# Kernel optimization log

Hardware: AMD Instinct MI355X
Metric: run time of the kernel (lower is better)

The kernel has to match this reference:

```python
import jax, jax.numpy as jnp
import numpy as np

N = 50000   # nodes
D = 128     # hidden_dim
H = 8       # num_heads
DK = D // H # per-head dim
E = 1600000 # edges
L = 2       # n_layers
LN_EPS = 1e-5


def _layer_norm(x, g, b):
    m = jnp.mean(x, axis=-1, keepdims=True)
    v = jnp.mean(jnp.square(x - m), axis=-1, keepdims=True)
    return (x - m) * jax.lax.rsqrt(v + LN_EPS) * g + b


def _gt_layer(h, src, dst, Wq, bq, Wk, bk, Wv, bv, Wo, bo, W1, b1, W2, b2, g1, be1, g2, be2):
    n = h.shape[0]
    Q = (h @ Wq + bq).reshape(n, H, DK)
    K = (h @ Wk + bk).reshape(n, H, DK)
    V = (h @ Wv + bv).reshape(n, H, DK)
    # per-edge scaled dot-product score: K[src] . Q[dst]
    score = jnp.einsum('ehd,ehd->eh', K[src], Q[dst]) / np.sqrt(DK)
    score = jnp.exp(jnp.clip(score, -5.0, 5.0))            # [E,H]
    wV = jax.ops.segment_sum(V[src] * score[:, :, None], dst, num_segments=n)  # [N,H,DK]
    z = jax.ops.segment_sum(score, dst, num_segments=n)    # [N,H]
    attn = wV / (z[:, :, None] + 1e-6)                     # possible_empty-safe softmax
    h_att = attn.reshape(n, D) @ Wo + bo
    h = _layer_norm(h + h_att, g1, be1)                    # residual + LN
    ffn = jax.nn.relu(h @ W1 + b1) @ W2 + b2
    h = _layer_norm(h + ffn, g2, be2)                      # residual + LN
    return h


def setup_inputs() -> dict:
    key = jax.random.key(0)
    ks = jax.random.split(key, 16)
    s = 1.0 / np.sqrt(D)
    s2 = 1.0 / np.sqrt(2 * D)
    w = lambda k, shape, sc: jax.random.normal(k, shape, jnp.float32) * sc
    return {
        'h':   jax.random.normal(ks[0], (N, D), jnp.float32),
        'src': jax.random.randint(ks[1], (E,), 0, N),
        'dst': jax.random.randint(ks[2], (E,), 0, N),
        'Wq': w(ks[3], (L, D, D), s), 'bq': jnp.zeros((L, D), jnp.float32),
        'Wk': w(ks[4], (L, D, D), s), 'bk': jnp.zeros((L, D), jnp.float32),
        'Wv': w(ks[5], (L, D, D), s), 'bv': jnp.zeros((L, D), jnp.float32),
        'Wo': w(ks[6], (L, D, D), s), 'bo': jnp.zeros((L, D), jnp.float32),
        'W1': w(ks[7], (L, D, 2 * D), s), 'b1': jnp.zeros((L, 2 * D), jnp.float32),
        'W2': w(ks[8], (L, 2 * D, D), s2), 'b2': jnp.zeros((L, D), jnp.float32),
        'ln1_g': jnp.ones((L, D), jnp.float32), 'ln1_b': jnp.zeros((L, D), jnp.float32),
        'ln2_g': jnp.ones((L, D), jnp.float32), 'ln2_b': jnp.zeros((L, D), jnp.float32),
    }


def reference(h, src, dst, Wq, bq, Wk, bk, Wv, bv, Wo, bo, W1, b1, W2, b2, ln1_g, ln1_b, ln2_g, ln2_b):
    for l in range(L):
        h = _gt_layer(h, src, dst, Wq[l], bq[l], Wk[l], bk[l], Wv[l], bv[l],
                      Wo[l], bo[l], W1[l], b1[l], W2[l], b2[l],
                      ln1_g[l], ln1_b[l], ln2_g[l], ln2_b[l])
    return h
```

## Files before the change

kernel.cpp:

```cpp
#include <hip/hip_runtime.h>

#define NN 50000
#define DD 128
#define HH 8
#define EE 1600000
#define LL 2

typedef unsigned short u16;
typedef __attribute__((ext_vector_type(8))) __bf16 bf16x8;
typedef __attribute__((ext_vector_type(4))) float f32x4;
typedef __attribute__((ext_vector_type(2))) float f32x2;

__device__ __forceinline__ float bf2f(u16 u){
    return __uint_as_float(((unsigned int)u) << 16);
}
__device__ __forceinline__ u16 f2bf(float f){
    unsigned int x = __float_as_uint(f);
    x = x + 0x7fff + ((x >> 16) & 1);
    return (u16)(x >> 16);
}

__device__ __forceinline__ void async16(const u16* g, u16* l){
    __builtin_amdgcn_global_load_lds(
        (const __attribute__((address_space(1))) unsigned int*)(const void*)g,
        (__attribute__((address_space(3))) unsigned int*)(void*)l, 16, 0, 0);
}

#define FILL_SUB 128
#define PREP_BLOCKS (1024 + 6250 + 384 + 768)

__global__ __launch_bounds__(256) void prep_kernel(
        const int* __restrict__ dst, int* __restrict__ cnt,
        const float* __restrict__ h_in, u16* __restrict__ hb,
        const float* __restrict__ Wq, const float* __restrict__ Wk, const float* __restrict__ Wv,
        const float* __restrict__ bq, const float* __restrict__ bk, const float* __restrict__ bv,
        u16* __restrict__ WtQKV, float* __restrict__ bQKV,
        const float* __restrict__ Wo, const float* __restrict__ W1, const float* __restrict__ W2,
        u16* __restrict__ WtO, u16* __restrict__ WtF1, u16* __restrict__ WtF2){
    int b = blockIdx.x;
    if (b < 1024){
        int slice = b & 7;
        int sub = b >> 3;
        int lo = slice * (NN / 8), hi = lo + (NN / 8);
        for (int e = sub * 256 + threadIdx.x; e < EE; e += FILL_SUB * 256){
            int d = dst[e];
            if (d >= lo && d < hi) atomicAdd(&cnt[d], 1);
        }
        return;
    }
    b -= 1024;
    if (b < 6250){
        int i = b * 256 + threadIdx.x;
        if (i < NN * DD / 4){
            float4 v = ((const float4*)h_in)[i];
            ushort4 o;
            o.x = f2bf(v.x); o.y = f2bf(v.y); o.z = f2bf(v.z); o.w = f2bf(v.w);
            ((ushort4*)hb)[i] = o;
        }
        return;
    }
    b -= 6250;
    if (b < 384){
        int l = b / 192;
        int idx = (b % 192) * 256 + threadIdx.x;
        if (idx < 384 * 128){
            int n = idx >> 7, k = idx & 127;
            const float* W = (n < 128) ? Wq : (n < 256) ? Wk : Wv;
            int nc = n & 127;
            WtQKV[(size_t)l * 384 * 128 + idx] = f2bf(W[(size_t)l * 128 * 128 + k * 128 + nc]);
            if (k == 0){
                const float* bb = (n < 128) ? bq : (n < 256) ? bk : bv;
                bQKV[l * 384 + n] = bb[l * 128 + nc];
            }
        }
        return;
    }
    b -= 384;
    {
        int which = b / 256;
        int rem = b % 256;
        int l = rem / 128;
        int idx = (rem % 128) * 256 + threadIdx.x;
        const float* in; u16* out; int R, C;
        if (which == 0){ in = Wo; out = WtO; R = 128; C = 128; }
        else if (which == 1){ in = W1; out = WtF1; R = 128; C = 256; }
        else { in = W2; out = WtF2; R = 256; C = 128; }
        int total = R * C;
        if (idx < total){
            size_t mat = (size_t)l * total;
            int r = idx / C, c = idx % C;
            out[mat + (size_t)c * R + r] = f2bf(in[mat + idx]);
        }
    }
}

__global__ __launch_bounds__(1024) void scan_kernel(const int* __restrict__ cnt,
                                                    int* __restrict__ offs, int* __restrict__ cur){
    __shared__ int wsum[16];
    __shared__ int carry_s;
    __shared__ int ctot_s;
    int t = threadIdx.x, lane = t & 63, w = t >> 6;
    if (t == 0){ offs[0] = 0; cur[0] = 0; carry_s = 0; }
    __syncthreads();
    const int N4 = NN / 4;
    for (int base = 0; base < N4; base += 1024){
        int i4 = base + t;
        int4 x = (i4 < N4) ? ((const int4*)cnt)[i4] : make_int4(0, 0, 0, 0);
        int s1 = x.x, s2 = s1 + x.y, s3 = s2 + x.z, s4 = s3 + x.w;
        int v = s4;
        #pragma unroll
        for (int d = 1; d < 64; d <<= 1){ int u = __shfl_up(v, d); if (lane >= d) v += u; }
        if (lane == 63) wsum[w] = v;
        __syncthreads();
        if (t < 16){
            int sv = wsum[t];
            int iv = sv;
            #pragma unroll
            for (int d = 1; d < 16; d <<= 1){ int u = __shfl_up(iv, d); if (t >= d) iv += u; }
            wsum[t] = iv - sv;
            if (t == 15) ctot_s = iv;
        }
        __syncthreads();
        int excl = carry_s + wsum[w] + (v - s4);
        if (i4 < N4){
            int o = 4 * i4;
            offs[o + 1] = excl + s1;  cur[o + 1] = excl + s1;
            offs[o + 2] = excl + s2;  cur[o + 2] = excl + s2;
            offs[o + 3] = excl + s3;  cur[o + 3] = excl + s3;
            offs[o + 4] = excl + s4;  cur[o + 4] = excl + s4;
        }
        __syncthreads();
        if (t == 0) carry_s += ctot_s;
        __syncthreads();
    }
}

__global__ __launch_bounds__(256) void fill_kernel(const int* __restrict__ src, const int* __restrict__ dst,
                                                   int* __restrict__ cur, int* __restrict__ srcs){
    int slice = blockIdx.x & 7;
    int sub = blockIdx.x >> 3;
    int lo = slice * (NN / 8), hi = lo + (NN / 8);
    for (int e = sub * 256 + threadIdx.x; e < EE; e += FILL_SUB * 256){
        int d = dst[e];
        if (d >= lo && d < hi){
            int p = atomicAdd(&cur[d], 1);
            srcs[p] = src[e];
        }
    }
}

#define BM 128
#define LDC 136

__device__ __forceinline__ void stage_tile(const u16* __restrict__ A, const u16* __restrict__ Wt,
                                           u16* As, u16* Bs, int M, int K, int m0, int n0, int k0,
                                           int w, int lane){
    int lr = lane >> 3;
    int swz = ((lane & 7) ^ lr) * 8;
    #pragma unroll
    for (int p = 0; p < 4; p++){
        int s = p * 4 + w;
        int ga = m0 + s * 8 + lr;
        if (ga >= M) ga = M - 1;
        async16(A + (size_t)ga * K + k0 + swz, As + s * 512);
        async16(Wt + (size_t)(n0 + s * 8 + lr) * K + k0 + swz, Bs + s * 512);
    }
}

__device__ __forceinline__ void mfma_tiles(const u16* As, const u16* Bs, f32x4 (&acc)[4][4],
                                           int wm, int wn, int l15, int hi){
    #pragma unroll
    for (int ks = 0; ks < 2; ks++){
        bf16x8 a[4], b[4];
        int ca = ((ks * 4 + hi) ^ (l15 & 7)) * 8;
        #pragma unroll
        for (int i = 0; i < 4; i++){
            a[i] = *(const bf16x8*)(As + (wm * 64 + i * 16 + l15) * 64 + ca);
            b[i] = *(const bf16x8*)(Bs + (wn * 64 + i * 16 + l15) * 64 + ca);
        }
        #pragma unroll
        for (int mi = 0; mi < 4; mi++)
            #pragma unroll
            for (int ni = 0; ni < 4; ni++)
                acc[mi][ni] = __builtin_amdgcn_mfma_f32_16x16x32_bf16(a[mi], b[ni], acc[mi][ni], 0, 0, 0);
    }
}

#define GEMM_LOOP(K)                                                          \
    for (int k0 = 0; k0 < (K); k0 += 64){                                     \
        __syncthreads();                                                      \
        stage_tile(A, Wt, As, Bs, M, (K), m0, n0, k0, w, lane);               \
        asm volatile("s_waitcnt vmcnt(0)" ::: "memory");                      \
        __syncthreads();                                                      \
        mfma_tiles(As, Bs, acc, wm, wn, l15, hi);                             \
    }

__global__ __launch_bounds__(256) void gemm_qkv(const u16* __restrict__ A, const u16* __restrict__ Wt,
                                                const float* __restrict__ bias,
                                                u16* __restrict__ Qb, u16* __restrict__ Kb,
                                                unsigned char* __restrict__ Vb, int M){
    __shared__ __align__(16) char smem[128 * LDC * 2];
    u16* As = (u16*)smem;
    u16* Bs = As + 8192;
    u16* Cs = (u16*)smem;

    int tid = threadIdx.x;
    int m0 = blockIdx.x * BM, n0 = blockIdx.y * 128;
    int lane = tid & 63, w = tid >> 6;
    int wm = w >> 1, wn = w & 1;
    int l15 = lane & 15, hi = lane >> 4;

    f32x4 acc[4][4];
    #pragma unroll
    for (int mi = 0; mi < 4; mi++)
        #pragma unroll
        for (int ni = 0; ni < 4; ni++)
            acc[mi][ni] = (f32x4){0.f, 0.f, 0.f, 0.f};

    GEMM_LOOP(128)

    __syncthreads();
    #pragma unroll
    for (int mi = 0; mi < 4; mi++)
        #pragma unroll
        for (int ni = 0; ni < 4; ni++){
            int col = wn * 64 + ni * 16 + l15;
            float bval = bias[n0 + col];
            #pragma unroll
            for (int j = 0; j < 4; j++){
                int rl = wm * 64 + mi * 16 + hi * 4 + j;
                Cs[rl * LDC + col] = f2bf(acc[mi][ni][j] + bval);
            }
        }
    __syncthreads();
    int qrow = tid >> 4, quad = tid & 15;
    if (n0 < 256){
        u16* Tb = (n0 == 0) ? Qb : Kb;
        #pragma unroll
        for (int p = 0; p < 8; p++){
            int rl = p * 16 + qrow;
            int gr = m0 + rl;
            if (gr < M){
                uint4 v = *(const uint4*)(&Cs[rl * LDC + quad * 8]);
                *(uint4*)(Tb + (size_t)gr * 128 + quad * 8) = v;
            }
        }
    } else {
        #pragma unroll
        for (int p = 0; p < 8; p++){
            int rl = p * 16 + qrow;
            int gr = m0 + rl;
            if (gr < M){
                uint4 v = *(const uint4*)(&Cs[rl * LDC + quad * 8]);
                float f0 = bf2f((u16)(v.x & 0xffff)), f1 = bf2f((u16)(v.x >> 16));
                float f2 = bf2f((u16)(v.y & 0xffff)), f3 = bf2f((u16)(v.y >> 16));
                float f4 = bf2f((u16)(v.z & 0xffff)), f5 = bf2f((u16)(v.z >> 16));
                float f6 = bf2f((u16)(v.w & 0xffff)), f7 = bf2f((u16)(v.w >> 16));
                unsigned int w0 = __builtin_amdgcn_cvt_pk_fp8_f32(f0, f1, 0u, false);
                w0 = __builtin_amdgcn_cvt_pk_fp8_f32(f2, f3, w0, true);
                unsigned int w1 = __builtin_amdgcn_cvt_pk_fp8_f32(f4, f5, 0u, false);
                w1 = __builtin_amdgcn_cvt_pk_fp8_f32(f6, f7, w1, true);
                *(uint2*)(Vb + (size_t)gr * 128 + quad * 8) = make_uint2(w0, w1);
            }
        }
    }
}

__global__ __launch_bounds__(256) void tail_kernel(const u16* __restrict__ att,
                                                   const u16* __restrict__ WtO, const float* __restrict__ bo,
                                                   const u16* __restrict__ resid,
                                                   const float* __restrict__ g1, const float* __restrict__ b1v,
                                                   const u16* __restrict__ W1t, const float* __restrict__ b1f,
                                                   const u16* __restrict__ W2t, const float* __restrict__ b2f,
                                                   const float* __restrict__ g2, const float* __restrict__ b2v,
                                                   u16* __restrict__ out_bf, float* __restrict__ out_f,
                                                   int M){
    __shared__ __align__(16) u16 h1c[8192];
    __shared__ __align__(16) u16 mid[16384];
    __shared__ __align__(16) u16 Bs[8192];
    __shared__ float ps[2][64];
    __shared__ float pss[2][64];
    u16* AsO = mid;

    int tid = threadIdx.x, lane = tid & 63, w = tid >> 6;
    int l15 = lane & 15, hi = lane >> 4;
    int wm = w >> 1, wn = w & 1;
    int m0 = blockIdx.x * 64;
    int lr = lane >> 3;
    int swz = ((lane & 7) ^ lr) * 8;

    f32x4 acc0[2][4];
    #pragma unroll
    for (int mi = 0; mi < 2; mi++)
        #pragma unroll
        for (int ni = 0; ni < 4; ni++)
            acc0[mi][ni] = (f32x4){0.f, 0.f, 0.f, 0.f};

    for (int kh = 0; kh < 2; kh++){
        __syncthreads();
        #pragma unroll
        for (int p = 0; p < 2; p++){
            int s = p * 4 + w;
            int ga = m0 + s * 8 + lr;
            if (ga >= M) ga = M - 1;
            async16(att + (size_t)ga * 128 + kh * 64 + swz, AsO + s * 512);
        }
        #pragma unroll
        for (int p = 0; p < 4; p++){
            int s = p * 4 + w;
            int row = s * 8 + lr;
            async16(WtO + (size_t)row * 128 + kh * 64 + swz, Bs + s * 512);
        }
        asm volatile("s_waitcnt vmcnt(0)" ::: "memory");
        __syncthreads();
        #pragma unroll
        for (int ks = 0; ks < 2; ks++){
            int ca = ((ks * 4 + hi) ^ (l15 & 7)) * 8;
            bf16x8 a[2], bb[4];
            #pragma unroll
            for (int i = 0; i < 2; i++)
                a[i] = *(const bf16x8*)(AsO + (wm * 32 + i * 16 + l15) * 64 + ca);
            #pragma unroll
            for (int i = 0; i < 4; i++)
                bb[i] = *(const bf16x8*)(Bs + (wn * 64 + i * 16 + l15) * 64 + ca);
            #pragma unroll
            for (int mi = 0; mi < 2; mi++)
                #pragma unroll
                for (int ni = 0; ni < 4; ni++)
                    acc0[mi][ni] = __builtin_amdgcn_mfma_f32_16x16x32_bf16(a[mi], bb[ni], acc0[mi][ni], 0, 0, 0);
        }
    }

    {
        float gc[4], bc[4], bv[4];
        #pragma unroll
        for (int ni = 0; ni < 4; ni++){
            int col = wn * 64 + ni * 16 + l15;
            gc[ni] = g1[col]; bc[ni] = b1v[col]; bv[ni] = bo[col];
        }
        #pragma unroll
        for (int mi = 0; mi < 2; mi++)
            #pragma unroll
            for (int j = 0; j < 4; j++){
                int row = wm * 32 + mi * 16 + hi * 4 + j;
                int gr = m0 + row;
                float s = 0.f, ss = 0.f;
                #pragma unroll
                for (int ni = 0; ni < 4; ni++){
                    int col = wn * 64 + ni * 16 + l15;
                    float x = acc0[mi][ni][j] + bv[ni];
                    if (gr < M) x += bf2f(resid[(size_t)gr * 128 + col]);
                    acc0[mi][ni][j] = x;
                    s += x; ss += x * x;
                }
                #pragma unroll
                for (int d = 1; d < 16; d <<= 1){
                    s  += __shfl_xor(s, d);
                    ss += __shfl_xor(ss, d);
                }
                if (l15 == 0){ ps[wn][row] = s; pss[wn][row] = ss; }
            }
        __syncthreads();
        #pragma unroll
        for (int mi = 0; mi < 2; mi++)
            #pragma unroll
            for (int j = 0; j < 4; j++){
                int row = wm * 32 + mi * 16 + hi * 4 + j;
                float s = ps[0][row] + ps[1][row];
                float ss = pss[0][row] + pss[1][row];
                float mean = s * (1.f / 128.f);
                float var = ss * (1.f / 128.f) - mean * mean;
                float r = rsqrtf(var + 1e-5f);
                #pragma unroll
                for (int ni = 0; ni < 4; ni++){
                    int kcol = ni * 16 + l15;
                    float o = (acc0[mi][ni][j] - mean) * r * gc[ni] + bc[ni];
                    h1c[wn * 4096 + row * 64 + (((kcol >> 3) ^ (row & 7)) * 8 + (kcol & 7))] = f2bf(o);
                }
            }
    }

    f32x4 acc1[2][2][4];
    #pragma unroll
    for (int nh = 0; nh < 2; nh++)
        #pragma unroll
        for (int mi = 0; mi < 2; mi++)
            #pragma unroll
            for (int ni = 0; ni < 4; ni++)
                acc1[nh][mi][ni] = (f32x4){0.f, 0.f, 0.f, 0.f};

    for (int nh = 0; nh < 2; nh++){
        for (int kh = 0; kh < 2; kh++){
            __syncthreads();
            #pragma unroll
            for (int p = 0; p < 4; p++){
                int s = p * 4 + w;
                int row = s * 8 + lr;
                async16(W1t + (size_t)(nh * 128 + row) * 128 + kh * 64 + swz, Bs + s * 512);
            }
            asm volatile("s_waitcnt vmcnt(0)" ::: "memory");
            __syncthreads();
            #pragma unroll
            for (int ks = 0; ks < 2; ks++){
                int ca = ((ks * 4 + hi) ^ (l15 & 7)) * 8;
                bf16x8 a[2], bb[4];
                #pragma unroll
                for (int i = 0; i < 2; i++)
                    a[i] = *(const bf16x8*)(h1c + kh * 4096 + (wm * 32 + i * 16 + l15) * 64 + ca);
                #pragma unroll
                for (int i = 0; i < 4; i++)
                    bb[i] = *(const bf16x8*)(Bs + (wn * 64 + i * 16 + l15) * 64 + ca);
                #pragma unroll
                for (int mi = 0; mi < 2; mi++)
                    #pragma unroll
                    for (int ni = 0; ni < 4; ni++)
                        acc1[nh][mi][ni] = __builtin_amdgcn_mfma_f32_16x16x32_bf16(a[mi], bb[ni], acc1[nh][mi][ni], 0, 0, 0);
            }
        }
    }
    __syncthreads();
    #pragma unroll
    for (int nh = 0; nh < 2; nh++)
        #pragma unroll
        for (int ni = 0; ni < 4; ni++){
            float bv = b1f[nh * 128 + wn * 64 + ni * 16 + l15];
            int kcol = ni * 16 + l15;
            int chunk = nh * 2 + wn;
            #pragma unroll
            for (int mi = 0; mi < 2; mi++)
                #pragma unroll
                for (int j = 0; j < 4; j++){
                    int row = wm * 32 + mi * 16 + hi * 4 + j;
                    float v = fmaxf(acc1[nh][mi][ni][j] + bv, 0.f);
                    mid[chunk * 4096 + row * 64 + (((kcol >> 3) ^ (row & 7)) * 8 + (kcol & 7))] = f2bf(v);
                }
        }

    f32x4 acc2[2][4];
    #pragma unroll
    for (int mi = 0; mi < 2; mi++)
        #pragma unroll
        for (int ni = 0; ni < 4; ni++)
            acc2[mi][ni] = (f32x4){0.f, 0.f, 0.f, 0.f};

    for (int kt = 0; kt < 4; kt++){
        __syncthreads();
        #pragma unroll
        for (int p = 0; p < 4; p++){
            int s = p * 4 + w;
            int row = s * 8 + lr;
            async16(W2t + (size_t)row * 256 + kt * 64 + swz, Bs + s * 512);
        }
        asm volatile("s_waitcnt vmcnt(0)" ::: "memory");
        __syncthreads();
        #pragma unroll
        for (int ks = 0; ks < 2; ks++){
            int ca = ((ks * 4 + hi) ^ (l15 & 7)) * 8;
            bf16x8 a[2], bb[4];
            #pragma unroll
            for (int i = 0; i < 2; i++)
                a[i] = *(const bf16x8*)(mid + kt * 4096 + (wm * 32 + i * 16 + l15) * 64 + ca);
            #pragma unroll
            for (int i = 0; i < 4; i++)
                bb[i] = *(const bf16x8*)(Bs + (wn * 64 + i * 16 + l15) * 64 + ca);
            #pragma unroll
            for (int mi = 0; mi < 2; mi++)
                #pragma unroll
                for (int ni = 0; ni < 4; ni++)
                    acc2[mi][ni] = __builtin_amdgcn_mfma_f32_16x16x32_bf16(a[mi], bb[ni], acc2[mi][ni], 0, 0, 0);
        }
    }

    float gc2[4], bc2[4], bv2[4];
    #pragma unroll
    for (int ni = 0; ni < 4; ni++){
        int col = wn * 64 + ni * 16 + l15;
        gc2[ni] = g2[col]; bc2[ni] = b2v[col]; bv2[ni] = b2f[col];
    }
    __syncthreads();
    #pragma unroll
    for (int mi = 0; mi < 2; mi++)
        #pragma unroll
        for (int j = 0; j < 4; j++){
            int row = wm * 32 + mi * 16 + hi * 4 + j;
            float s = 0.f, ss = 0.f;
            #pragma unroll
            for (int ni = 0; ni < 4; ni++){
                int kcol = ni * 16 + l15;
                float h1v = bf2f(h1c[wn * 4096 + row * 64 + (((kcol >> 3) ^ (row & 7)) * 8 + (kcol & 7))]);
                float x = acc2[mi][ni][j] + bv2[ni] + h1v;
                acc2[mi][ni][j] = x;
                s += x; ss += x * x;
            }
            #pragma unroll
            for (int d = 1; d < 16; d <<= 1){
                s  += __shfl_xor(s, d);
                ss += __shfl_xor(ss, d);
            }
            if (l15 == 0){ ps[wn][row] = s; pss[wn][row] = ss; }
        }
    __syncthreads();

    #pragma unroll
    for (int mi = 0; mi < 2; mi++)
        #pragma unroll
        for (int j = 0; j < 4; j++){
            int row = wm * 32 + mi * 16 + hi * 4 + j;
            int gr = m0 + row;
            if (gr >= M) continue;
            float s = ps[0][row] + ps[1][row];
            float ss = pss[0][row] + pss[1][row];
            float mean = s * (1.f / 128.f);
            float var = ss * (1.f / 128.f) - mean * mean;
            float r = rsqrtf(var + 1e-5f);
            #pragma unroll
            for (int ni = 0; ni < 4; ni++){
                int col = wn * 64 + ni * 16 + l15;
                float o = (acc2[mi][ni][j] - mean) * r * gc2[ni] + bc2[ni];
                if (out_f) out_f[(size_t)gr * 128 + col] = o;
                else       out_bf[(size_t)gr * 128 + col] = f2bf(o);
            }
        }
}

__global__ __launch_bounds__(256) void edge_attn_kernel(const u16* __restrict__ Qb,
                                                        const u16* __restrict__ Kb,
                                                        const unsigned char* __restrict__ Vb,
                                                        const int* __restrict__ srcs,
                                                        const int* __restrict__ offs,
                                                        u16* __restrict__ att){
    int n = blockIdx.x * 4 + (threadIdx.x >> 6);
    if (n >= NN) return;
    int lane = threadIdx.x & 63;
    int laneh = lane & 31;
    int half = lane >> 5;

    float q0, q1, q2, q3;
    {
        uint2 qv = *(const uint2*)(Qb + (size_t)n * 128 + 4 * laneh);
        q0 = bf2f((u16)(qv.x & 0xffff)); q1 = bf2f((u16)(qv.x >> 16));
        q2 = bf2f((u16)(qv.y & 0xffff)); q3 = bf2f((u16)(qv.y >> 16));
    }
    const u16* kbase = Kb + 4 * laneh;
    const unsigned char* vbase = Vb + 4 * laneh;

    float w0 = 0.f, w1 = 0.f, w2 = 0.f, w3 = 0.f, z = 0.f;
    const float CS = 0.25f * 1.44269504f;

    auto proc = [&](uint2 kk, unsigned int vv, float gate){
        float k0 = bf2f((u16)(kk.x & 0xffff)), k1 = bf2f((u16)(kk.x >> 16));
        float k2 = bf2f((u16)(kk.y & 0xffff)), k3 = bf2f((u16)(kk.y >> 16));
        float p = q0 * k0 + q1 * k1 + q2 * k2 + q3 * k3;
        p += __shfl_xor(p, 1);
        p += __shfl_xor(p, 2);
        p = __builtin_amdgcn_fmed3f(p, -20.f, 20.f);
        float sc = __builtin_amdgcn_exp2f(p * CS) * gate;
        f32x2 vl = __builtin_amdgcn_cvt_pk_f32_fp8(vv, false);
        f32x2 vh = __builtin_amdgcn_cvt_pk_f32_fp8(vv, true);
        w0 += sc * vl[0]; w1 += sc * vl[1]; w2 += sc * vh[0]; w3 += sc * vh[1];
        z += sc;
    };

    int e0 = offs[n], e1 = offs[n + 1];
    int i = e0;
    for (; i + 15 < e1; i += 16){
        int s[8];
        #pragma unroll
        for (int u = 0; u < 8; u++) s[u] = srcs[i + 2 * u + half];
        uint2 kk[8];
        unsigned int vv[8];
        #pragma unroll
        for (int u = 0; u < 8; u++){
            kk[u] = *(const uint2*)(kbase + (size_t)s[u] * 128);
            vv[u] = *(const unsigned int*)(vbase + (size_t)s[u] * 128);
        }
        #pragma unroll
        for (int u = 0; u < 8; u++) proc(kk[u], vv[u], 1.f);
    }
    for (; i + 1 < e1; i += 2){
        int s = srcs[i + half];
        proc(*(const uint2*)(kbase + (size_t)s * 128),
             *(const unsigned int*)(vbase + (size_t)s * 128), 1.f);
    }
    if (i < e1){
        int s = srcs[i];
        proc(*(const uint2*)(kbase + (size_t)s * 128),
             *(const unsigned int*)(vbase + (size_t)s * 128), half ? 0.f : 1.f);
    }

    w0 += __shfl_xor(w0, 32); w1 += __shfl_xor(w1, 32);
    w2 += __shfl_xor(w2, 32); w3 += __shfl_xor(w3, 32);
    z  += __shfl_xor(z, 32);

    if (!half){
        float inv = 1.f / (z + 1e-6f);
        unsigned int oA = (unsigned int)f2bf(w0 * inv) | ((unsigned int)f2bf(w1 * inv) << 16);
        unsigned int oB = (unsigned int)f2bf(w2 * inv) | ((unsigned int)f2bf(w3 * inv) << 16);
        *(uint2*)(att + (size_t)n * DD + 4 * laneh) = make_uint2(oA, oB);
    }
}

extern "C" void kernel_launch(void* const* d_in, const int* in_sizes, int n_in,
                              void* d_out, int out_size, void* d_ws, size_t ws_size,
                              hipStream_t stream){
    const float* h_in = (const float*)d_in[0];
    const int* src  = (const int*)d_in[1];
    const int* dst  = (const int*)d_in[2];
    const float* Wq = (const float*)d_in[3];
    const float* bq = (const float*)d_in[4];
    const float* Wk = (const float*)d_in[5];
    const float* bk = (const float*)d_in[6];
    const float* Wv = (const float*)d_in[7];
    const float* bv = (const float*)d_in[8];
    const float* Wo = (const float*)d_in[9];
    const float* bo = (const float*)d_in[10];
    const float* W1 = (const float*)d_in[11];
    const float* b1 = (const float*)d_in[12];
    const float* W2 = (const float*)d_in[13];
    const float* b2 = (const float*)d_in[14];
    const float* ln1_g = (const float*)d_in[15];
    const float* ln1_b = (const float*)d_in[16];
    const float* ln2_g = (const float*)d_in[17];
    const float* ln2_b = (const float*)d_in[18];
    float* outp = (float*)d_out;

    char* ws = (char*)d_ws;
    auto alloc = [&](size_t bytes) -> char* {
        char* p = ws;
        ws += (bytes + 255) & ~(size_t)255;
        return p;
    };
    int* cnt   = (int*)alloc((size_t)NN * 4);
    int* offs  = (int*)alloc((size_t)(NN + 1) * 4);
    int* cur   = (int*)alloc((size_t)(NN + 1) * 4);
    int* srcs  = (int*)alloc((size_t)EE * 4);
    u16* WtQKV = (u16*)alloc((size_t)LL * 384 * 128 * 2);
    float* bQKV = (float*)alloc((size_t)LL * 384 * 4);
    u16* WtO   = (u16*)alloc((size_t)LL * 128 * 128 * 2);
    u16* WtF1  = (u16*)alloc((size_t)LL * 256 * 128 * 2);
    u16* WtF2  = (u16*)alloc((size_t)LL * 128 * 256 * 2);
    u16* hb    = (u16*)alloc((size_t)NN * DD * 2);
    u16* Qb    = (u16*)alloc((size_t)NN * 128 * 2);
    u16* Kb    = (u16*)alloc((size_t)NN * 128 * 2);
    unsigned char* Vb = (unsigned char*)alloc((size_t)NN * 128);
    u16* att   = (u16*)alloc((size_t)NN * DD * 2);
    u16* hmid  = (u16*)alloc((size_t)NN * DD * 2);

    hipMemsetAsync(cnt, 0, (size_t)NN * 4, stream);
    prep_kernel<<<PREP_BLOCKS, 256, 0, stream>>>(dst, cnt, h_in, hb,
                                                 Wq, Wk, Wv, bq, bk, bv, WtQKV, bQKV,
                                                 Wo, W1, W2, WtO, WtF1, WtF2);
    scan_kernel<<<1, 1024, 0, stream>>>(cnt, offs, cur);
    fill_kernel<<<8 * FILL_SUB, 256, 0, stream>>>(src, dst, cur, srcs);

    const int MB = (NN + BM - 1) / BM;
    const int MB64 = (NN + 63) / 64;
    const u16* hcur = hb;
    for (int l = 0; l < LL; l++){
        gemm_qkv<<<dim3(MB, 3), 256, 0, stream>>>(hcur, WtQKV + (size_t)l * 384 * 128,
                                                  bQKV + l * 384, Qb, Kb, Vb, NN);
        edge_attn_kernel<<<NN / 4, 256, 0, stream>>>(Qb, Kb, Vb, srcs, offs, att);
        if (l == LL - 1)
            tail_kernel<<<MB64, 256, 0, stream>>>(att, WtO + (size_t)l * 128 * 128, bo + l * 128,
                                                  hcur, ln1_g + l * 128, ln1_b + l * 128,
                                                  WtF1 + (size_t)l * 256 * 128, b1 + l * 256,
                                                  WtF2 + (size_t)l * 128 * 256, b2 + l * 128,
                                                  ln2_g + l * 128, ln2_b + l * 128,
                                                  nullptr, outp, NN);
        else
            tail_kernel<<<MB64, 256, 0, stream>>>(att, WtO + (size_t)l * 128 * 128, bo + l * 128,
                                                  hcur, ln1_g + l * 128, ln1_b + l * 128,
                                                  WtF1 + (size_t)l * 256 * 128, b1 + l * 256,
                                                  WtF2 + (size_t)l * 128 * 256, b2 + l * 128,
                                                  ln2_g + l * 128, ln2_b + l * 128,
                                                  hmid, nullptr, NN);
        hcur = hmid;
    }
}
```

Measured before the change: 455.9 us.

## Fuse next layer's QKV projection into layer-one tail kernel

The first layer's tail kernel now keeps its bf16 LayerNorm output tile in shared memory and immediately computes the second layer's Q, K and V projections (with FP8 packing for V), writing them directly. This removes the separate gemm_qkv launch for layer two and the re-read of the hidden state from global memory. In exchange the tail kernel gets longer and uses more registers and shared-memory traffic, and it adds six serialized weight-chunk loads per block with synchronisation between them.

```diff
diff --git a/kernel.cpp b/kernel.cpp
--- a/kernel.cpp
+++ b/kernel.cpp
@@ -274,6 +274,9 @@
                                                    const u16* __restrict__ W2t, const float* __restrict__ b2f,
                                                    const float* __restrict__ g2, const float* __restrict__ b2v,
                                                    u16* __restrict__ out_bf, float* __restrict__ out_f,
+                                                   const u16* __restrict__ WtQn, const float* __restrict__ bQn,
+                                                   u16* __restrict__ Qb, u16* __restrict__ Kb,
+                                                   unsigned char* __restrict__ Vb,
                                                    int M){
     __shared__ __align__(16) u16 h1c[8192];
     __shared__ __align__(16) u16 mid[16384];
@@ -281,6 +284,7 @@
     __shared__ float ps[2][64];
     __shared__ float pss[2][64];
     u16* AsO = mid;
+    u16* Cs  = mid;
 
     int tid = threadIdx.x, lane = tid & 63, w = tid >> 6;
     int l15 = lane & 15, hi = lane >> 4;
@@ -518,9 +522,102 @@
                 int col = wn * 64 + ni * 16 + l15;
                 float o = (acc2[mi][ni][j] - mean) * r * gc2[ni] + bc2[ni];
                 if (out_f) out_f[(size_t)gr * 128 + col] = o;
-                else       out_bf[(size_t)gr * 128 + col] = f2bf(o);
-            }
-        }
+                else {
+                    u16 ob = f2bf(o);
+                    out_bf[(size_t)gr * 128 + col] = ob;
+                    if (Qb){
+                        int kcol = ni * 16 + l15;
+                        h1c[wn * 4096 + row * 64 + (((kcol >> 3) ^ (row & 7)) * 8 + (kcol & 7))] = ob;
+                    }
+                }
+            }
+        }
+
+    if (!Qb) return;
+    __syncthreads();
+    for (int nc = 0; nc < 6; nc++){
+        __syncthreads();
+        #pragma unroll
+        for (int kh = 0; kh < 2; kh++)
+            #pragma unroll
+            for (int p = 0; p < 2; p++){
+                int s = p * 4 + w;
+                int row = s * 8 + lr;
+                async16(WtQn + (size_t)(nc * 64 + row) * 128 + kh * 64 + swz,
+                        Bs + kh * 4096 + s * 512);
+            }
+        asm volatile("s_waitcnt vmcnt(0)" ::: "memory");
+        __syncthreads();
+        f32x4 aq[2][2];
+        #pragma unroll
+        for (int mi = 0; mi < 2; mi++)
+            #pragma unroll
+            for (int ni = 0; ni < 2; ni++)
+                aq[mi][ni] = (f32x4){0.f, 0.f, 0.f, 0.f};
+        #pragma unroll
+        for (int kh = 0; kh < 2; kh++)
+            #pragma unroll
+            for (int ks = 0; ks < 2; ks++){
+                int ca = ((ks * 4 + hi) ^ (l15 & 7)) * 8;
+                bf16x8 a[2], bb[2];
+                #pragma unroll
+                for (int i = 0; i < 2; i++){
+                    a[i]  = *(const bf16x8*)(h1c + kh * 4096 + (wm * 32 + i * 16 + l15) * 64 + ca);
+                    bb[i] = *(const bf16x8*)(Bs  + kh * 4096 + (wn * 32 + i * 16 + l15) * 64 + ca);
+                }
+                #pragma unroll
+                for (int mi = 0; mi < 2; mi++)
+                    #pragma unroll
+                    for (int ni = 0; ni < 2; ni++)
+                        aq[mi][ni] = __builtin_amdgcn_mfma_f32_16x16x32_bf16(a[mi], bb[ni], aq[mi][ni], 0, 0, 0);
+            }
+        #pragma unroll
+        for (int mi = 0; mi < 2; mi++)
+            #pragma unroll
+            for (int ni = 0; ni < 2; ni++){
+                int col = wn * 32 + ni * 16 + l15;
+                float bval = bQn[nc * 64 + col];
+                #pragma unroll
+                for (int j = 0; j < 4; j++){
+                    int row = wm * 32 + mi * 16 + hi * 4 + j;
+                    Cs[row * 68 + col] = f2bf(aq[mi][ni][j] + bval);
+                }
+            }
+        __syncthreads();
+        int srow = tid >> 3, scol = (tid & 7) * 8;
+        if (nc < 4){
+            u16* Tb = (nc < 2) ? Qb : Kb;
+            int cbase = (nc & 1) * 64;
+            #pragma unroll
+            for (int pass = 0; pass < 2; pass++){
+                int row = pass * 32 + srow;
+                int gr = m0 + row;
+                if (gr < M){
+                    uint4 v = *(const uint4*)(&Cs[row * 68 + scol]);
+                    *(uint4*)(Tb + (size_t)gr * 128 + cbase + scol) = v;
+                }
+            }
+        } else {
+            int cbase = (nc & 1) * 64;
+            #pragma unroll
+            for (int pass = 0; pass < 2; pass++){
+                int row = pass * 32 + srow;
+                int gr = m0 + row;
+                if (gr < M){
+                    uint4 v = *(const uint4*)(&Cs[row * 68 + scol]);
+                    float f0 = bf2f((u16)(v.x & 0xffff)), f1 = bf2f((u16)(v.x >> 16));
+                    float f2 = bf2f((u16)(v.y & 0xffff)), f3 = bf2f((u16)(v.y >> 16));
+                    float f4 = bf2f((u16)(v.z & 0xffff)), f5 = bf2f((u16)(v.z >> 16));
+                    float f6 = bf2f((u16)(v.w & 0xffff)), f7 = bf2f((u16)(v.w >> 16));
+                    unsigned int w0 = __builtin_amdgcn_cvt_pk_fp8_f32(f0, f1, 0u, false);
+                    w0 = __builtin_amdgcn_cvt_pk_fp8_f32(f2, f3, w0, true);
+                    unsigned int w1 = __builtin_amdgcn_cvt_pk_fp8_f32(f4, f5, 0u, false);
+                    w1 = __builtin_amdgcn_cvt_pk_fp8_f32(f6, f7, w1, true);
+                    *(uint2*)(Vb + (size_t)gr * 128 + cbase + scol) = make_uint2(w0, w1);
+                }
+            }
+        }
+    }
 }
 
 __global__ __launch_bounds__(256) void edge_attn_kernel(const u16* __restrict__ Qb,
@@ -655,25 +752,20 @@
 
     const int MB = (NN + BM - 1) / BM;
     const int MB64 = (NN + 63) / 64;
-    const u16* hcur = hb;
-    for (int l = 0; l < LL; l++){
-        gemm_qkv<<<dim3(MB, 3), 256, 0, stream>>>(hcur, WtQKV + (size_t)l * 384 * 128,
-                                                  bQKV + l * 384, Qb, Kb, Vb, NN);
-        edge_attn_kernel<<<NN / 4, 256, 0, stream>>>(Qb, Kb, Vb, srcs, offs, att);
-        if (l == LL - 1)
-            tail_kernel<<<MB64, 256, 0, stream>>>(att, WtO + (size_t)l * 128 * 128, bo + l * 128,
-                                                  hcur, ln1_g + l * 128, ln1_b + l * 128,
-                                                  WtF1 + (size_t)l * 256 * 128, b1 + l * 256,
-                                                  WtF2 + (size_t)l * 128 * 256, b2 + l * 128,
-                                                  ln2_g + l * 128, ln2_b + l * 128,
-                                                  nullptr, outp, NN);
-        else
-            tail_kernel<<<MB64, 256, 0, stream>>>(att, WtO + (size_t)l * 128 * 128, bo + l * 128,
-                                                  hcur, ln1_g + l * 128, ln1_b + l * 128,
-                                                  WtF1 + (size_t)l * 256 * 128, b1 + l * 256,
-                                                  WtF2 + (size_t)l * 128 * 256, b2 + l * 128,
-                                                  ln2_g + l * 128, ln2_b + l * 128,
-                                                  hmid, nullptr, NN);
-        hcur = hmid;
-    }
-}
+
+    gemm_qkv<<<dim3(MB, 3), 256, 0, stream>>>(hb, WtQKV, bQKV, Qb, Kb, Vb, NN);
+    edge_attn_kernel<<<NN / 4, 256, 0, stream>>>(Qb, Kb, Vb, srcs, offs, att);
+    tail_kernel<<<MB64, 256, 0, stream>>>(att, WtO, bo, hb, ln1_g, ln1_b,
+                                          WtF1, b1, WtF2, b2, ln2_g, ln2_b,
+                                          hmid, nullptr,
+                                          WtQKV + (size_t)384 * 128, bQKV + 384,
+                                          Qb, Kb, Vb, NN);
+    edge_attn_kernel<<<NN / 4, 256, 0, stream>>>(Qb, Kb, Vb, srcs, offs, att);
+    tail_kernel<<<MB64, 256, 0, stream>>>(att, WtO + (size_t)128 * 128, bo + 128,
+                                          hmid, ln1_g + 128, ln1_b + 128,
+                                          WtF1 + (size_t)256 * 128, b1 + 256,
+                                          WtF2 + (size_t)128 * 256, b2 + 128,
+                                          ln2_g + 128, ln2_b + 128,
+                                          nullptr, outp,
+                                          nullptr, nullptr, nullptr, nullptr, nullptr, NN);
+}
```

New measurement: 534.7 us. 1.17x slower.
